# Kernel tuning notes

Measured on AMD Instinct MI355X. Metric: run time of the kernel, lower is better.

The kernel has to match this reference:

```python
import jax, jax.numpy as jnp
import numpy as np
from jax import lax

T, B, E = 4096, 8, 512


def setup_inputs() -> dict:
    key = jax.random.key(0)
    k1, k2, k3 = jax.random.split(key, 3)
    x = jax.random.normal(k1, (T, B, E), dtype=jnp.float32)
    raw_pos_beta = jax.random.normal(k2, (E,), dtype=jnp.float32)
    raw_neg_beta = jax.random.normal(k3, (E,), dtype=jnp.float32)
    return {"x": x, "raw_pos_beta": raw_pos_beta, "raw_neg_beta": raw_neg_beta}


def reference(x, raw_pos_beta, raw_neg_beta):
    # pos/neg split EMA. The torch module computes out[t] = sum_{s<=t} beta^(t-s) u[s]
    # via a length-T depthwise conv; that is exactly the linear recurrence
    # mem[t] = beta * mem[t-1] + u[t], which we run as an O(T) scan.
    pos_beta = jax.nn.sigmoid(raw_pos_beta)  # [E]
    neg_beta = jax.nn.sigmoid(raw_neg_beta)  # [E]
    x_pos = jnp.where(x >= 0, x, 0.0) * (1.0 - pos_beta)  # [T,B,E]
    x_neg = jnp.where(x <= 0, x, 0.0) * (1.0 - neg_beta)  # [T,B,E]
    u = jnp.stack([x_pos, x_neg], axis=-1)                # [T,B,E,2]
    beta = jnp.stack([pos_beta, neg_beta], axis=-1)       # [E,2]

    def step(carry, u_t):
        new = beta * carry + u_t  # [B,E,2]
        return new, new

    init = jnp.zeros(u.shape[1:], dtype=x.dtype)
    _, mem2 = lax.scan(step, init, u)  # [T,B,E,2]
    return mem2[..., 0] + mem2[..., 1]  # [T,B,E]
```

## Files before the change

kernel.cpp:

```cpp
#include <hip/hip_runtime.h>


#define T_DIM 4096
#define B_DIM 8
#define E_DIM 512
#define CHUNK_L 16
#define NCHUNK (T_DIM / CHUNK_L)
#define BE (B_DIM * E_DIM)

__device__ __forceinline__ float sigmoidf_(float x) { return 1.0f / (1.0f + __expf(-x)); }

__global__ __launch_bounds__(256) void ParallelDLIEMA_17789754541002_kernel(
        const float* __restrict__ x,
        const float* __restrict__ rp,
        const float* __restrict__ rn,
        float* __restrict__ out) {
    int gtid = blockIdx.x * 256 + threadIdx.x;
    int e4 = gtid & 127;
    int b  = (gtid >> 7) & 7;
    int c  = gtid >> 10;
    int e  = e4 * 4;

    float4 rp4 = *(const float4*)(rp + e);
    float4 rn4 = *(const float4*)(rn + e);
    float bp[4] = {sigmoidf_(rp4.x), sigmoidf_(rp4.y), sigmoidf_(rp4.z), sigmoidf_(rp4.w)};
    float bn[4] = {sigmoidf_(rn4.x), sigmoidf_(rn4.y), sigmoidf_(rn4.z), sigmoidf_(rn4.w)};

    float fp4[4] = {0.f, 0.f, 0.f, 0.f};
    float fn4[4] = {0.f, 0.f, 0.f, 0.f};
    int base = c * CHUNK_L * BE + b * E_DIM + e;
    #pragma unroll
    for (int k = 0; k < CHUNK_L; k++) {
        float4 xv = *(const float4*)(x + base + k * BE);
        float f[4] = {xv.x, xv.y, xv.z, xv.w};
        #pragma unroll
        for (int j = 0; j < 4; j++) {
            fp4[j] = bp[j] * fp4[j] + fmaxf(f[j], 0.f) * (1.0f - bp[j]);
            fn4[j] = bn[j] * fn4[j] + fminf(f[j], 0.f) * (1.0f - bn[j]);
        }
    }
    *(float4*)(out + base + 0 * BE) = make_float4(fp4[0], fp4[1], fp4[2], fp4[3]);
    *(float4*)(out + base + 1 * BE) = make_float4(fn4[0], fn4[1], fn4[2], fn4[3]);
}

__global__ __launch_bounds__(256) void k_carry(const float* __restrict__ rp,
                                               const float* __restrict__ rn,
                                               float* __restrict__ out) {
    int gtid = blockIdx.x * 256 + threadIdx.x;
    int e = gtid & 511;
    int b = (gtid >> 9) & 7;
    int s = gtid >> 12;
    float beta = sigmoidf_(s ? rn[e] : rp[e]);
    float bl = beta * beta; bl = bl * bl; bl = bl * bl; bl = bl * bl;

    float* p = out + s * BE + b * E_DIM + e;
    float carry = 0.f;
    for (int g = 0; g < NCHUNK / 16; g++) {
        float fv[16];
        #pragma unroll
        for (int u = 0; u < 16; u++) fv[u] = p[(g * 16 + u) * (CHUNK_L * BE)];
        #pragma unroll
        for (int u = 0; u < 16; u++) {
            p[(g * 16 + u) * (CHUNK_L * BE)] = carry;
            carry = bl * carry + fv[u];
        }
    }
}

__global__ __launch_bounds__(256) void k_out(const float* __restrict__ x,
                                             const float* __restrict__ rp,
                                             const float* __restrict__ rn,
                                             float* __restrict__ out) {
    int gtid = blockIdx.x * 256 + threadIdx.x;
    int e4 = gtid & 127;
    int b  = (gtid >> 7) & 7;
    int c  = gtid >> 10;
    int e  = e4 * 4;

    float4 rp4 = *(const float4*)(rp + e);
    float4 rn4 = *(const float4*)(rn + e);
    float bp[4] = {sigmoidf_(rp4.x), sigmoidf_(rp4.y), sigmoidf_(rp4.z), sigmoidf_(rp4.w)};
    float bn[4] = {sigmoidf_(rn4.x), sigmoidf_(rn4.y), sigmoidf_(rn4.z), sigmoidf_(rn4.w)};

    int base = c * CHUNK_L * BE + b * E_DIM + e;
    float4 cp = *(const float4*)(out + base + 0 * BE);
    float4 cn = *(const float4*)(out + base + 1 * BE);
    float lp[4] = {cp.x, cp.y, cp.z, cp.w};
    float ln[4] = {cn.x, cn.y, cn.z, cn.w};

    #pragma unroll
    for (int k = 0; k < CHUNK_L; k++) {
        float4 xv = *(const float4*)(x + base + k * BE);
        float f[4] = {xv.x, xv.y, xv.z, xv.w};
        float o[4];
        #pragma unroll
        for (int j = 0; j < 4; j++) {
            lp[j] = bp[j] * lp[j] + fmaxf(f[j], 0.f) * (1.0f - bp[j]);
            ln[j] = bn[j] * ln[j] + fminf(f[j], 0.f) * (1.0f - bn[j]);
            o[j] = lp[j] + ln[j];
        }
        *(float4*)(out + base + k * BE) = make_float4(o[0], o[1], o[2], o[3]);
    }
}

extern "C" void kernel_launch(void* const* d_in, const int* in_sizes, int n_in,
                              void* d_out, int out_size, void* d_ws, size_t ws_size,
                              hipStream_t stream) {
    const float* x  = (const float*)d_in[0];
    const float* rp = (const float*)d_in[1];
    const float* rn = (const float*)d_in[2];
    float* out = (float*)d_out;

    ParallelDLIEMA_17789754541002_kernel<<<1024, 256, 0, stream>>>(x, rp, rn, out);
    k_carry<<<32, 256, 0, stream>>>(rp, rn, out);
    k_out<<<1024, 256, 0, stream>>>(x, rp, rn, out);
}
```

Before: 136.6 us.

## Fuse three-phase chunked scan into one cooperative kernel with register-held inputs

Merges the chunk-local scan, the carry propagation and the output pass into one cooperative kernel separated by grid-wide syncs. The 64 input values per thread stay in registers, so x is read from global memory once instead of twice, and chunk finals go to a compact workspace. The cost is two grid.sync barriers, a carry phase that runs on only 8192 threads while the rest wait, and higher register pressure from the 64-float array. If the cooperative launch fails, it falls back to the original three-kernel path.

```diff
diff --git a/kernel.cpp b/kernel.cpp
--- a/kernel.cpp
+++ b/kernel.cpp
@@ -1,4 +1,7 @@
 #include <hip/hip_runtime.h>
+#include <hip/hip_cooperative_groups.h>
+
+namespace cg = cooperative_groups;
 
 
 #define T_DIM 4096
@@ -7,8 +10,89 @@
 #define CHUNK_L 16
 #define NCHUNK (T_DIM / CHUNK_L)
 #define BE (B_DIM * E_DIM)
+#define FINALS (NCHUNK * B_DIM * E_DIM)
 
 __device__ __forceinline__ float sigmoidf_(float x) { return 1.0f / (1.0f + __expf(-x)); }
+
+__global__ __launch_bounds__(256, 4) void ema_fused(
+        const float* __restrict__ x,
+        const float* __restrict__ rp,
+        const float* __restrict__ rn,
+        float* __restrict__ out,
+        float* __restrict__ ws) {
+    cg::grid_group grid = cg::this_grid();
+
+    int gtid = blockIdx.x * 256 + threadIdx.x;
+    int e4 = gtid & 127;
+    int b  = (gtid >> 7) & 7;
+    int c  = gtid >> 10;
+    int e  = e4 * 4;
+
+    float4 rp4 = *(const float4*)(rp + e);
+    float4 rn4 = *(const float4*)(rn + e);
+    float bp[4] = {sigmoidf_(rp4.x), sigmoidf_(rp4.y), sigmoidf_(rp4.z), sigmoidf_(rp4.w)};
+    float bn[4] = {sigmoidf_(rn4.x), sigmoidf_(rn4.y), sigmoidf_(rn4.z), sigmoidf_(rn4.w)};
+
+    float xr[64];
+    float fp4[4] = {0.f, 0.f, 0.f, 0.f};
+    float fn4[4] = {0.f, 0.f, 0.f, 0.f};
+    int base = c * CHUNK_L * BE + b * E_DIM + e;
+    #pragma unroll
+    for (int k = 0; k < CHUNK_L; k++) {
+        float4 xv = *(const float4*)(x + base + k * BE);
+        xr[4*k+0] = xv.x; xr[4*k+1] = xv.y; xr[4*k+2] = xv.z; xr[4*k+3] = xv.w;
+        #pragma unroll
+        for (int j = 0; j < 4; j++) {
+            float f = xr[4*k+j];
+            fp4[j] = bp[j] * fp4[j] + fmaxf(f, 0.f) * (1.0f - bp[j]);
+            fn4[j] = bn[j] * fn4[j] + fminf(f, 0.f) * (1.0f - bn[j]);
+        }
+    }
+    int fi = (c * B_DIM + b) * E_DIM + e;
+    *(float4*)(ws + fi)          = make_float4(fp4[0], fp4[1], fp4[2], fp4[3]);
+    *(float4*)(ws + FINALS + fi) = make_float4(fn4[0], fn4[1], fn4[2], fn4[3]);
+
+    grid.sync();
+
+    if (gtid < 2 * BE) {
+        int ee = gtid & 511;
+        int bb = (gtid >> 9) & 7;
+        int s  = gtid >> 12;
+        float beta = sigmoidf_(s ? rn[ee] : rp[ee]);
+        float bl = beta * beta; bl = bl * bl; bl = bl * bl; bl = bl * bl;
+        float* p = ws + s * FINALS + bb * E_DIM + ee;
+        float carry = 0.f;
+        for (int g = 0; g < NCHUNK / 16; g++) {
+            float fv[16];
+            #pragma unroll
+            for (int u = 0; u < 16; u++) fv[u] = p[(g * 16 + u) * BE];
+            #pragma unroll
+            for (int u = 0; u < 16; u++) {
+                p[(g * 16 + u) * BE] = carry;
+                carry = bl * carry + fv[u];
+            }
+        }
+    }
+
+    grid.sync();
+
+    float4 cp = *(const float4*)(ws + fi);
+    float4 cn = *(const float4*)(ws + FINALS + fi);
+    float lp[4] = {cp.x, cp.y, cp.z, cp.w};
+    float ln[4] = {cn.x, cn.y, cn.z, cn.w};
+    #pragma unroll
+    for (int k = 0; k < CHUNK_L; k++) {
+        float o[4];
+        #pragma unroll
+        for (int j = 0; j < 4; j++) {
+            float f = xr[4*k+j];
+            lp[j] = bp[j] * lp[j] + fmaxf(f, 0.f) * (1.0f - bp[j]);
+            ln[j] = bn[j] * ln[j] + fminf(f, 0.f) * (1.0f - bn[j]);
+            o[j] = lp[j] + ln[j];
+        }
+        *(float4*)(out + base + k * BE) = make_float4(o[0], o[1], o[2], o[3]);
+    }
+}
 
 __global__ __launch_bounds__(256) void ParallelDLIEMA_17789754541002_kernel(
         const float* __restrict__ x,
@@ -110,8 +194,14 @@
     const float* rp = (const float*)d_in[1];
     const float* rn = (const float*)d_in[2];
     float* out = (float*)d_out;
-
-    ParallelDLIEMA_17789754541002_kernel<<<1024, 256, 0, stream>>>(x, rp, rn, out);
-    k_carry<<<32, 256, 0, stream>>>(rp, rn, out);
-    k_out<<<1024, 256, 0, stream>>>(x, rp, rn, out);
-}
+    float* ws  = (float*)d_ws;
+
+    void* args[] = {(void*)&x, (void*)&rp, (void*)&rn, (void*)&out, (void*)&ws};
+    hipError_t err = hipLaunchCooperativeKernel((void*)ema_fused, dim3(1024),
+                                                dim3(256), args, 0, stream);
+    if (err != hipSuccess) {
+        ParallelDLIEMA_17789754541002_kernel<<<1024, 256, 0, stream>>>(x, rp, rn, out);
+        k_carry<<<32, 256, 0, stream>>>(rp, rn, out);
+        k_out<<<1024, 256, 0, stream>>>(x, rp, rn, out);
+    }
+}
```

After: 418.1 us. 206% more time.
